# Optimization experiments

Measured on AMD Instinct MI355X. Metric: run time of the kernel, lower is better.

Reference implementation:

```python
import jax, jax.numpy as jnp
import numpy as np

VOCAB = 1024
CTX = 8
D = VOCAB * CTX  # flattened one-hot dim = Linear in/out features
BATCH = 1024


def setup_inputs() -> dict:
    key = jax.random.key(0)
    k1, k2, k3 = jax.random.split(key, 3)
    x = jax.random.randint(k1, (BATCH, CTX), 0, VOCAB)
    # nn.Linear params: weight (out, in) = (D, D), bias (D,)
    W = jax.random.normal(k2, (D, D), dtype=jnp.float32) * 0.02
    b = jax.random.normal(k3, (D,), dtype=jnp.float32) * 0.02
    return {"x": x, "W": W, "b": b}


def reference(x, W, b):
    B, T = x.shape
    # one_hot(x).view(B, T*V) @ W.T + b  ==  sum_t W[:, t*V + x[:,t]] + b
    flat_idx = jnp.arange(T) * VOCAB + x  # [B, T], values in [0, D)
    # gather weight columns: [D, B, T], sum over context positions -> [D, B]
    gathered = jnp.take(W, flat_idx, axis=1)
    logits_flat = gathered.sum(axis=-1).T + b  # [B, D]
    return logits_flat.reshape(B, T, VOCAB)
```

## Files before the change

### kernel.cpp

```cpp
#include <hip/hip_runtime.h>

#define VOCAB 1024
#define CTX 8
#define DDIM 8192
#define BATCH 1024

__global__ __launch_bounds__(256) void p1_gather(const int* __restrict__ x,
                                                 const float* __restrict__ W,
                                                 const float* __restrict__ b,
                                                 float* __restrict__ outT) {
    __shared__ float row[DDIM];
    const int d   = blockIdx.x;
    const int tid = threadIdx.x;
    const float* wrow = W + (size_t)d * DDIM;

#pragma unroll
    for (int it = 0; it < DDIM / (256 * 4); ++it) {
        const int e = (it * 256 + tid) * 4;
        const float4 v = *reinterpret_cast<const float4*>(wrow + e);
        *reinterpret_cast<float4*>(&row[e]) = v;
    }
    __syncthreads();

    const float bias = b[d];
    const int ibase = tid * 4;
    float4 res;
#pragma unroll
    for (int k = 0; k < 4; ++k) {
        const int i = ibase + k;
        const int4 xa = *reinterpret_cast<const int4*>(x + i * CTX);
        const int4 xb = *reinterpret_cast<const int4*>(x + i * CTX + 4);
        float s = row[0 * VOCAB + xa.x] + row[1 * VOCAB + xa.y] +
                  row[2 * VOCAB + xa.z] + row[3 * VOCAB + xa.w] +
                  row[4 * VOCAB + xb.x] + row[5 * VOCAB + xb.y] +
                  row[6 * VOCAB + xb.z] + row[7 * VOCAB + xb.w];
        (&res.x)[k] = s + bias;
    }
    *reinterpret_cast<float4*>(outT + (size_t)d * BATCH + ibase) = res;
}

__global__ __launch_bounds__(256) void p2_transpose(const float* __restrict__ outT,
                                                    float* __restrict__ out) {
    __shared__ float tile[64][65];
    const int i0  = (blockIdx.x & 15) * 64;
    const int d0  = (blockIdx.x >> 4) * 64;
    const int tid = threadIdx.x;
    const int c   = tid & 15;
    const int r   = tid >> 4;

#pragma unroll
    for (int p = 0; p < 4; ++p) {
        const int dl = r + p * 16;
        const float4 v = *reinterpret_cast<const float4*>(
            outT + (size_t)(d0 + dl) * BATCH + i0 + c * 4);
        tile[c * 4 + 0][dl] = v.x;
        tile[c * 4 + 1][dl] = v.y;
        tile[c * 4 + 2][dl] = v.z;
        tile[c * 4 + 3][dl] = v.w;
    }
    __syncthreads();

#pragma unroll
    for (int p = 0; p < 4; ++p) {
        const int il = r + p * 16;
        float4 v;
        v.x = tile[il][c * 4 + 0];
        v.y = tile[il][c * 4 + 1];
        v.z = tile[il][c * 4 + 2];
        v.w = tile[il][c * 4 + 3];
        *reinterpret_cast<float4*>(out + (size_t)(i0 + il) * DDIM + d0 + c * 4) = v;
    }
}

__global__ __launch_bounds__(256) void fallback_direct(const int* __restrict__ x,
                                                       const float* __restrict__ W,
                                                       const float* __restrict__ b,
                                                       float* __restrict__ out) {
    const int i  = blockIdx.y;
    const int d0 = (blockIdx.x * 256 + threadIdx.x) * 4;
    if (d0 >= DDIM) return;
    int c[CTX];
#pragma unroll
    for (int t = 0; t < CTX; ++t) c[t] = t * VOCAB + x[i * CTX + t];
    float4 res;
#pragma unroll
    for (int j = 0; j < 4; ++j) {
        float s = b[d0 + j];
#pragma unroll
        for (int t = 0; t < CTX; ++t) s += W[(size_t)(d0 + j) * DDIM + c[t]];
        (&res.x)[j] = s;
    }
    *reinterpret_cast<float4*>(out + (size_t)i * DDIM + d0) = res;
}

extern "C" void kernel_launch(void* const* d_in, const int* in_sizes, int n_in,
                              void* d_out, int out_size, void* d_ws, size_t ws_size,
                              hipStream_t stream) {
    const int*   x = (const int*)d_in[0];
    const float* W = (const float*)d_in[1];
    const float* b = (const float*)d_in[2];
    float*     out = (float*)d_out;

    const size_t need = (size_t)DDIM * BATCH * sizeof(float);
    if (ws_size >= need) {
        float* outT = (float*)d_ws;
        hipLaunchKernelGGL(p1_gather, dim3(DDIM), dim3(256), 0, stream,
                           x, W, b, outT);
        hipLaunchKernelGGL(p2_transpose, dim3(128 * 16), dim3(256), 0, stream,
                           outT, out);
    } else {
        hipLaunchKernelGGL(fallback_direct, dim3(DDIM / 1024, BATCH), dim3(256),
                           0, stream, x, W, b, out);
    }
}
```

Measured before the change: 381.3 us.

## Fuse gather and transpose into one double-buffered LDS kernel

Replaces the two-kernel scheme (gather into a transposed workspace, then a tiled transpose) with a single kernel. Each block stages 16 rows of W into a double-buffered LDS area using direct global-to-LDS loads. Each of its 1024 threads owns one batch row, gathers the 8 indexed entries per W row, and writes 16 contiguous outputs. This removes the 32 MB workspace write and re-read plus the second launch. In exchange it uses 64 KB of LDS per block, 1024-thread blocks and only 512 blocks, and the output stores are 64-byte chunks strided by a full row per thread.

```diff
diff --git a/kernel.cpp b/kernel.cpp
--- a/kernel.cpp
+++ b/kernel.cpp
@@ -4,93 +4,87 @@
 #define CTX 8
 #define DDIM 8192
 #define BATCH 1024
+#define RDIM 16
 
-__global__ __launch_bounds__(256) void p1_gather(const int* __restrict__ x,
-                                                 const float* __restrict__ W,
-                                                 const float* __restrict__ b,
-                                                 float* __restrict__ outT) {
-    __shared__ float row[DDIM];
-    const int d   = blockIdx.x;
+__global__ __launch_bounds__(1024, 8) void fused_gather(
+    const int* __restrict__ x, const float* __restrict__ W,
+    const float* __restrict__ b, float* __restrict__ out) {
+    __shared__ __align__(16) float lds[2][DDIM];
     const int tid = threadIdx.x;
-    const float* wrow = W + (size_t)d * DDIM;
+    const int d0  = blockIdx.x * RDIM;
+
+#define STAGE(BUF, DD)                                                         \
+    {                                                                          \
+        const float* _src = W + (size_t)(d0 + (DD)) * DDIM + tid * 4;          \
+        __builtin_amdgcn_global_load_lds(                                      \
+            (const __attribute__((address_space(1))) void*)(_src),             \
+            (__attribute__((address_space(3))) void*)(&lds[(BUF)][tid * 4]),   \
+            16, 0, 0);                                                         \
+        __builtin_amdgcn_global_load_lds(                                      \
+            (const __attribute__((address_space(1))) void*)(_src + 4096),      \
+            (__attribute__((address_space(3))) void*)(&lds[(BUF)][4096 + tid * 4]), \
+            16, 0, 0);                                                         \
+    }
+
+    STAGE(0, 0)
+
+    const int4 xa = *reinterpret_cast<const int4*>(x + tid * CTX);
+    const int4 xb = *reinterpret_cast<const int4*>(x + tid * CTX + 4);
+    const int o0 = xa.x;
+    const int o1 = 1 * VOCAB + xa.y;
+    const int o2 = 2 * VOCAB + xa.z;
+    const int o3 = 3 * VOCAB + xa.w;
+    const int o4 = 4 * VOCAB + xb.x;
+    const int o5 = 5 * VOCAB + xb.y;
+    const int o6 = 6 * VOCAB + xb.z;
+    const int o7 = 7 * VOCAB + xb.w;
+
+    float acc[RDIM];
 
 #pragma unroll
-    for (int it = 0; it < DDIM / (256 * 4); ++it) {
-        const int e = (it * 256 + tid) * 4;
-        const float4 v = *reinterpret_cast<const float4*>(wrow + e);
-        *reinterpret_cast<float4*>(&row[e]) = v;
+    for (int dl = 0; dl < RDIM; ++dl) {
+        if (dl < RDIM - 1) {
+            STAGE((dl + 1) & 1, dl + 1)
+            asm volatile("s_waitcnt vmcnt(2)" ::: "memory");
+        } else {
+            asm volatile("s_waitcnt vmcnt(0)" ::: "memory");
+        }
+        __builtin_amdgcn_s_barrier();
+
+        const float* buf = &lds[dl & 1][0];
+        const float v0 = buf[o0];
+        const float v1 = buf[o1];
+        const float v2 = buf[o2];
+        const float v3 = buf[o3];
+        const float v4 = buf[o4];
+        const float v5 = buf[o5];
+        const float v6 = buf[o6];
+        const float v7 = buf[o7];
+        acc[dl] = ((v0 + v1) + (v2 + v3)) + ((v4 + v5) + (v6 + v7));
+
+        if (dl < RDIM - 1)
+            __builtin_amdgcn_s_barrier();
     }
-    __syncthreads();
+#undef STAGE
 
-    const float bias = b[d];
-    const int ibase = tid * 4;
-    float4 res;
-#pragma unroll
-    for (int k = 0; k < 4; ++k) {
-        const int i = ibase + k;
-        const int4 xa = *reinterpret_cast<const int4*>(x + i * CTX);
-        const int4 xb = *reinterpret_cast<const int4*>(x + i * CTX + 4);
-        float s = row[0 * VOCAB + xa.x] + row[1 * VOCAB + xa.y] +
-                  row[2 * VOCAB + xa.z] + row[3 * VOCAB + xa.w] +
-                  row[4 * VOCAB + xb.x] + row[5 * VOCAB + xb.y] +
-                  row[6 * VOCAB + xb.z] + row[7 * VOCAB + xb.w];
-        (&res.x)[k] = s + bias;
-    }
-    *reinterpret_cast<float4*>(outT + (size_t)d * BATCH + ibase) = res;
-}
-
-__global__ __launch_bounds__(256) void p2_transpose(const float* __restrict__ outT,
-                                                    float* __restrict__ out) {
-    __shared__ float tile[64][65];
-    const int i0  = (blockIdx.x & 15) * 64;
-    const int d0  = (blockIdx.x >> 4) * 64;
-    const int tid = threadIdx.x;
-    const int c   = tid & 15;
-    const int r   = tid >> 4;
-
-#pragma unroll
-    for (int p = 0; p < 4; ++p) {
-        const int dl = r + p * 16;
-        const float4 v = *reinterpret_cast<const float4*>(
-            outT + (size_t)(d0 + dl) * BATCH + i0 + c * 4);
-        tile[c * 4 + 0][dl] = v.x;
-        tile[c * 4 + 1][dl] = v.y;
-        tile[c * 4 + 2][dl] = v.z;
-        tile[c * 4 + 3][dl] = v.w;
-    }
-    __syncthreads();
-
-#pragma unroll
-    for (int p = 0; p < 4; ++p) {
-        const int il = r + p * 16;
-        float4 v;
-        v.x = tile[il][c * 4 + 0];
-        v.y = tile[il][c * 4 + 1];
-        v.z = tile[il][c * 4 + 2];
-        v.w = tile[il][c * 4 + 3];
-        *reinterpret_cast<float4*>(out + (size_t)(i0 + il) * DDIM + d0 + c * 4) = v;
-    }
-}
-
-__global__ __launch_bounds__(256) void fallback_direct(const int* __restrict__ x,
-                                                       const float* __restrict__ W,
-                                                       const float* __restrict__ b,
-                                                       float* __restrict__ out) {
-    const int i  = blockIdx.y;
-    const int d0 = (blockIdx.x * 256 + threadIdx.x) * 4;
-    if (d0 >= DDIM) return;
-    int c[CTX];
-#pragma unroll
-    for (int t = 0; t < CTX; ++t) c[t] = t * VOCAB + x[i * CTX + t];
-    float4 res;
-#pragma unroll
-    for (int j = 0; j < 4; ++j) {
-        float s = b[d0 + j];
-#pragma unroll
-        for (int t = 0; t < CTX; ++t) s += W[(size_t)(d0 + j) * DDIM + c[t]];
-        (&res.x)[j] = s;
-    }
-    *reinterpret_cast<float4*>(out + (size_t)i * DDIM + d0) = res;
+    const float4 bv0 = *reinterpret_cast<const float4*>(b + d0);
+    const float4 bv1 = *reinterpret_cast<const float4*>(b + d0 + 4);
+    const float4 bv2 = *reinterpret_cast<const float4*>(b + d0 + 8);
+    const float4 bv3 = *reinterpret_cast<const float4*>(b + d0 + 12);
+    float* orow = out + (size_t)tid * DDIM + d0;
+    float4 r;
+    r.x = acc[0] + bv0.x;  r.y = acc[1] + bv0.y;
+    r.z = acc[2] + bv0.z;  r.w = acc[3] + bv0.w;
+    reinterpret_cast<float4*>(orow)[0] = r;
+    r.x = acc[4] + bv1.x;  r.y = acc[5] + bv1.y;
+    r.z = acc[6] + bv1.z;  r.w = acc[7] + bv1.w;
+    reinterpret_cast<float4*>(orow)[1] = r;
+    r.x = acc[8] + bv2.x;  r.y = acc[9] + bv2.y;
+    r.z = acc[10] + bv2.z; r.w = acc[11] + bv2.w;
+    reinterpret_cast<float4*>(orow)[2] = r;
+    r.x = acc[12] + bv3.x; r.y = acc[13] + bv3.y;
+    r.z = acc[14] + bv3.z; r.w = acc[15] + bv3.w;
+    reinterpret_cast<float4*>(orow)[3] = r;
 }
 
 extern "C" void kernel_launch(void* const* d_in, const int* in_sizes, int n_in,
@@ -101,15 +95,6 @@
     const float* b = (const float*)d_in[2];
     float*     out = (float*)d_out;
 
-    const size_t need = (size_t)DDIM * BATCH * sizeof(float);
-    if (ws_size >= need) {
-        float* outT = (float*)d_ws;
-        hipLaunchKernelGGL(p1_gather, dim3(DDIM), dim3(256), 0, stream,
-                           x, W, b, outT);
-        hipLaunchKernelGGL(p2_transpose, dim3(128 * 16), dim3(256), 0, stream,
-                           outT, out);
-    } else {
-        hipLaunchKernelGGL(fallback_direct, dim3(DDIM / 1024, BATCH), dim3(256),
-                           0, stream, x, W, b, out);
-    }
+    hipLaunchKernelGGL(fused_gather, dim3(DDIM / RDIM), dim3(1024), 0, stream,
+                       x, W, b, out);
 }
```

New measurement: 441.0 us. 15.7% more time.
